# Optimization experiments

Hardware: AMD Instinct MI355X
Metric: run time of the kernel (lower is better)

The kernel has to match this reference:

```python
import jax, jax.numpy as jnp
import numpy as np

N = 50000
E = 800000
D = 64


def setup_inputs() -> dict:
    key = jax.random.key(0)
    k1, k2, k3, k4, k5, k6 = jax.random.split(key, 6)
    node_feats = jax.random.normal(k1, (N, D), dtype=jnp.float32)
    edge_feats = jax.random.normal(k2, (E, D), dtype=jnp.float32)
    src = jax.random.randint(k3, (E,), 0, N, dtype=jnp.int32)
    dst = jnp.sort(jax.random.randint(k4, (E,), 0, N, dtype=jnp.int32))
    # Linear(in_feats=D, out_feats=D) parameters (PyTorch default init scale)
    lim = 1.0 / np.sqrt(D)
    W = jax.random.uniform(k5, (D, D), minval=-lim, maxval=lim, dtype=jnp.float32)
    b = jax.random.uniform(k6, (D,), minval=-lim, maxval=lim, dtype=jnp.float32)
    return {"node_feats": node_feats, "edge_feats": edge_feats, "src": src,
            "dst": dst, "W": W, "b": b}


def reference(node_feats, edge_feats, src, dst, W, b):
    # u_add_e: per-edge message m_e = h_src(e) + h_e   [E, D]
    m = node_feats[src] + edge_feats
    # edge_softmax over edges grouped by destination node, per feature dim
    seg_max = jax.ops.segment_max(m, dst, num_segments=N)        # [N, D]
    seg_max = jnp.where(jnp.isfinite(seg_max), seg_max, 0.0)     # nodes w/o in-edges
    ex = jnp.exp(m - seg_max[dst])                               # [E, D]
    denom = jax.ops.segment_sum(ex, dst, num_segments=N)         # [N, D]
    a = ex / jnp.maximum(denom[dst], 1e-38)                      # [E, D]
    # weighted scatter-sum: h'_v = sum_{e->v} m_e * a_e
    agg = jax.ops.segment_sum(m * a, dst, num_segments=N)        # [N, D]
    # MLP + activation + residual (dropout=0, output_norm='none')
    out = jax.nn.relu(agg @ W.T + b) + node_feats
    return out
```

## Files before the change

### kernel.cpp

```cpp
#include <hip/hip_runtime.h>
#include <math.h>

#define DD 64
typedef float v4f __attribute__((ext_vector_type(4)));

__global__ __launch_bounds__(256) void prep_kernel(const int* __restrict__ dst,
                                                   int* __restrict__ row_start,
                                                   int N, int E) {
    int e = blockIdx.x * blockDim.x + threadIdx.x;
    if (e >= E) return;
    const int b = dst[e];
    const int a = (e == 0) ? -1 : dst[e - 1];
    for (int v = a + 1; v <= b; ++v) row_start[v] = e;
    if (e == E - 1) {
        for (int v = b + 1; v <= N; ++v) row_start[v] = E;
    }
}

__global__ __launch_bounds__(256) void fused_kernel(
    const float* __restrict__ node_feats,
    const float* __restrict__ edge_feats,
    const int*   __restrict__ src,
    const int*   __restrict__ row_start,
    const float* __restrict__ W,
    const float* __restrict__ bvec,
    float*       __restrict__ out,
    int N)
{
    __shared__ float rowbuf[4][DD];

    const int wave = threadIdx.x >> 6;
    const int lane = threadIdx.x & 63;
    const int grp  = lane >> 4;
    const int qd   = lane & 15;
    const int v = blockIdx.x * 4 + wave;
    if (v >= N) return;

    v4f wreg[16];
#pragma unroll
    for (int q = 0; q < 16; ++q)
        wreg[q] = ((const v4f*)W)[(size_t)lane * 16 + q];
    const float bj = bvec[lane];

    const int e0 = row_start[v];
    const int e1 = row_start[v + 1];

    const v4f* __restrict__ nf4 = (const v4f*)node_feats;
    const v4f* __restrict__ ef4 = (const v4f*)edge_feats;

    v4f se = {0.f, 0.f, 0.f, 0.f};
    v4f sm = {0.f, 0.f, 0.f, 0.f};

#define ACCUM(mv, valid)                                \
    {   v4f x;                                          \
        x.x = (valid) ? __expf((mv).x) : 0.f;           \
        x.y = (valid) ? __expf((mv).y) : 0.f;           \
        x.z = (valid) ? __expf((mv).z) : 0.f;           \
        x.w = (valid) ? __expf((mv).w) : 0.f;           \
        se += x;                                        \
        sm += (mv) * x;                                 \
    }

    for (int cb = e0; cb < e1; cb += 64) {
        const int li   = cb + lane;
        const int spre = src[li < e1 ? li : e0];
        const int cend = (cb + 64 < e1) ? (cb + 64) : e1;

        for (int eb = cb; eb < cend; eb += 16) {
            const int rb = eb - cb;
            const int sA = __shfl(spre, rb + grp,      64);
            const int sB = __shfl(spre, rb + 4  + grp, 64);
            const int sC = __shfl(spre, rb + 8  + grp, 64);
            const int sD = __shfl(spre, rb + 12 + grp, 64);

            const int eA = eb + grp,      eB = eb + 4 + grp;
            const int eC = eb + 8 + grp,  eD = eb + 12 + grp;
            const bool vA = eA < cend, vB = eB < cend;
            const bool vC = eC < cend, vD = eD < cend;
            const int cA = vA ? eA : e0, cB = vB ? eB : e0;
            const int cC = vC ? eC : e0, cD = vD ? eD : e0;

            const v4f gA = __builtin_nontemporal_load(ef4 + (size_t)cA * 16 + qd);
            const v4f gB = __builtin_nontemporal_load(ef4 + (size_t)cB * 16 + qd);
            const v4f gC = __builtin_nontemporal_load(ef4 + (size_t)cC * 16 + qd);
            const v4f gD = __builtin_nontemporal_load(ef4 + (size_t)cD * 16 + qd);
            const v4f nA = nf4[(size_t)sA * 16 + qd];
            const v4f nB = nf4[(size_t)sB * 16 + qd];
            const v4f nC = nf4[(size_t)sC * 16 + qd];
            const v4f nD = nf4[(size_t)sD * 16 + qd];

            const v4f mA = nA + gA;
            const v4f mB = nB + gB;
            const v4f mC = nC + gC;
            const v4f mD = nD + gD;
            ACCUM(mA, vA);
            ACCUM(mB, vB);
            ACCUM(mC, vC);
            ACCUM(mD, vD);
        }
    }
#undef ACCUM

    for (int off = 16; off < 64; off <<= 1) {
        se.x += __shfl_xor(se.x, off, 64);
        se.y += __shfl_xor(se.y, off, 64);
        se.z += __shfl_xor(se.z, off, 64);
        se.w += __shfl_xor(se.w, off, 64);
        sm.x += __shfl_xor(sm.x, off, 64);
        sm.y += __shfl_xor(sm.y, off, 64);
        sm.z += __shfl_xor(sm.z, off, 64);
        sm.w += __shfl_xor(sm.w, off, 64);
    }

    v4f a;
    a.x = sm.x / fmaxf(se.x, 1e-38f);
    a.y = sm.y / fmaxf(se.y, 1e-38f);
    a.z = sm.z / fmaxf(se.z, 1e-38f);
    a.w = sm.w / fmaxf(se.w, 1e-38f);

    if (grp == 0)
        *(v4f*)(&rowbuf[wave][qd * 4]) = a;
    asm volatile("s_waitcnt lgkmcnt(0)" ::: "memory");

    float acc = bj;
    const v4f* __restrict__ rp = (const v4f*)rowbuf[wave];
#pragma unroll
    for (int q = 0; q < 16; ++q) {
        const v4f av = rp[q];
        acc = fmaf(av.x, wreg[q].x, acc);
        acc = fmaf(av.y, wreg[q].y, acc);
        acc = fmaf(av.z, wreg[q].z, acc);
        acc = fmaf(av.w, wreg[q].w, acc);
    }
    const float res = node_feats[(size_t)v * DD + lane];
    out[(size_t)v * DD + lane] = fmaxf(acc, 0.f) + res;
}

extern "C" void kernel_launch(void* const* d_in, const int* in_sizes, int n_in,
                              void* d_out, int out_size, void* d_ws, size_t ws_size,
                              hipStream_t stream) {
    const float* node_feats = (const float*)d_in[0];
    const float* edge_feats = (const float*)d_in[1];
    const int*   src        = (const int*)  d_in[2];
    const int*   dst        = (const int*)  d_in[3];
    const float* W          = (const float*)d_in[4];
    const float* bvec       = (const float*)d_in[5];
    float*       out        = (float*)d_out;

    const int N = in_sizes[0] / DD;
    const int E = in_sizes[2];

    int* row_start = (int*)d_ws;

    {
        int blocks = (E + 255) / 256;
        prep_kernel<<<blocks, 256, 0, stream>>>(dst, row_start, N, E);
    }
    {
        int blocks = (N + 3) / 4;
        fused_kernel<<<blocks, 256, 0, stream>>>(node_feats, edge_feats, src,
                                                 row_start, W, bvec, out, N);
    }
}
```

Measured before the change: 376.3 us.

## Make fused kernel persistent with grid-stride nodes and prefetch next node's indices

Turns the fused aggregation kernel into a persistent grid-stride loop capped at 2048 blocks. Each wave loads W into registers once and reuses it across many nodes, and it prefetches row_start and the first src chunk for the next node while working on the current one. A launch-bounds occupancy hint is added. This amortizes the per-node W loads and hides index-load latency, at the cost of fewer resident waves and possible load imbalance across degree-varying nodes.

```diff
diff --git a/kernel.cpp b/kernel.cpp
--- a/kernel.cpp
+++ b/kernel.cpp
@@ -17,7 +17,7 @@
     }
 }
 
-__global__ __launch_bounds__(256) void fused_kernel(
+__global__ __launch_bounds__(256, 3) void fused_kernel(
     const float* __restrict__ node_feats,
     const float* __restrict__ edge_feats,
     const int*   __restrict__ src,
@@ -29,27 +29,33 @@
 {
     __shared__ float rowbuf[4][DD];
 
-    const int wave = threadIdx.x >> 6;
-    const int lane = threadIdx.x & 63;
-    const int grp  = lane >> 4;
-    const int qd   = lane & 15;
-    const int v = blockIdx.x * 4 + wave;
-    if (v >= N) return;
+    const int wave   = threadIdx.x >> 6;
+    const int lane   = threadIdx.x & 63;
+    const int grp    = lane >> 4;
+    const int qd     = lane & 15;
+    const int stride = gridDim.x * 4;
 
     v4f wreg[16];
 #pragma unroll
-    for (int q = 0; q < 16; ++q)
+    for (int q = 0; q < 16; ++q) {
         wreg[q] = ((const v4f*)W)[(size_t)lane * 16 + q];
+        asm volatile("" : "+v"(wreg[q]));
+    }
     const float bj = bvec[lane];
 
-    const int e0 = row_start[v];
-    const int e1 = row_start[v + 1];
+    int v = blockIdx.x * 4 + wave;
+    if (v >= N) return;
 
     const v4f* __restrict__ nf4 = (const v4f*)node_feats;
     const v4f* __restrict__ ef4 = (const v4f*)edge_feats;
 
-    v4f se = {0.f, 0.f, 0.f, 0.f};
-    v4f sm = {0.f, 0.f, 0.f, 0.f};
+    int e0 = row_start[v];
+    int e1 = row_start[v + 1];
+    int vn = v + stride;
+    int e0n = 0, e1n = 0;
+    if (vn < N) { e0n = row_start[vn]; e1n = row_start[vn + 1]; }
+    int li0 = e0 + lane;
+    int sc  = src[li0 < e1 ? li0 : (e1 > e0 ? e0 : 0)];
 
 #define ACCUM(mv, valid)                                \
     {   v4f x;                                          \
@@ -61,79 +67,100 @@
         sm += (mv) * x;                                 \
     }
 
-    for (int cb = e0; cb < e1; cb += 64) {
-        const int li   = cb + lane;
-        const int spre = src[li < e1 ? li : e0];
-        const int cend = (cb + 64 < e1) ? (cb + 64) : e1;
+    while (v < N) {
+        int spre_next = 0;
+        if (vn < N) {
+            const int lin = e0n + lane;
+            spre_next = src[lin < e1n ? lin : (e1n > e0n ? e0n : 0)];
+        }
+        const int v2 = vn + stride;
+        int e0nn = 0, e1nn = 0;
+        if (v2 < N) { e0nn = row_start[v2]; e1nn = row_start[v2 + 1]; }
 
-        for (int eb = cb; eb < cend; eb += 16) {
-            const int rb = eb - cb;
-            const int sA = __shfl(spre, rb + grp,      64);
-            const int sB = __shfl(spre, rb + 4  + grp, 64);
-            const int sC = __shfl(spre, rb + 8  + grp, 64);
-            const int sD = __shfl(spre, rb + 12 + grp, 64);
+        const float res = node_feats[(size_t)v * DD + lane];
 
-            const int eA = eb + grp,      eB = eb + 4 + grp;
-            const int eC = eb + 8 + grp,  eD = eb + 12 + grp;
-            const bool vA = eA < cend, vB = eB < cend;
-            const bool vC = eC < cend, vD = eD < cend;
-            const int cA = vA ? eA : e0, cB = vB ? eB : e0;
-            const int cC = vC ? eC : e0, cD = vD ? eD : e0;
+        v4f se = {0.f, 0.f, 0.f, 0.f};
+        v4f sm = {0.f, 0.f, 0.f, 0.f};
 
-            const v4f gA = __builtin_nontemporal_load(ef4 + (size_t)cA * 16 + qd);
-            const v4f gB = __builtin_nontemporal_load(ef4 + (size_t)cB * 16 + qd);
-            const v4f gC = __builtin_nontemporal_load(ef4 + (size_t)cC * 16 + qd);
-            const v4f gD = __builtin_nontemporal_load(ef4 + (size_t)cD * 16 + qd);
-            const v4f nA = nf4[(size_t)sA * 16 + qd];
-            const v4f nB = nf4[(size_t)sB * 16 + qd];
-            const v4f nC = nf4[(size_t)sC * 16 + qd];
-            const v4f nD = nf4[(size_t)sD * 16 + qd];
+        for (int cb = e0; cb < e1; cb += 64) {
+            const int li   = cb + lane;
+            const int spre = (cb == e0) ? sc
+                             : src[li < e1 ? li : e0];
+            const int cend = (cb + 64 < e1) ? (cb + 64) : e1;
 
-            const v4f mA = nA + gA;
-            const v4f mB = nB + gB;
-            const v4f mC = nC + gC;
-            const v4f mD = nD + gD;
-            ACCUM(mA, vA);
-            ACCUM(mB, vB);
-            ACCUM(mC, vC);
-            ACCUM(mD, vD);
+            for (int eb = cb; eb < cend; eb += 16) {
+                const int rb = eb - cb;
+                const int sA = __shfl(spre, rb + grp,      64);
+                const int sB = __shfl(spre, rb + 4  + grp, 64);
+                const int sC = __shfl(spre, rb + 8  + grp, 64);
+                const int sD = __shfl(spre, rb + 12 + grp, 64);
+
+                const int eA = eb + grp,      eB = eb + 4 + grp;
+                const int eC = eb + 8 + grp,  eD = eb + 12 + grp;
+                const bool vA = eA < cend, vB = eB < cend;
+                const bool vC = eC < cend, vD = eD < cend;
+                const int cA = vA ? eA : e0, cB = vB ? eB : e0;
+                const int cC = vC ? eC : e0, cD = vD ? eD : e0;
+
+                const v4f gA = __builtin_nontemporal_load(ef4 + (size_t)cA * 16 + qd);
+                const v4f gB = __builtin_nontemporal_load(ef4 + (size_t)cB * 16 + qd);
+                const v4f gC = __builtin_nontemporal_load(ef4 + (size_t)cC * 16 + qd);
+                const v4f gD = __builtin_nontemporal_load(ef4 + (size_t)cD * 16 + qd);
+                const v4f nA = nf4[(size_t)sA * 16 + qd];
+                const v4f nB = nf4[(size_t)sB * 16 + qd];
+                const v4f nC = nf4[(size_t)sC * 16 + qd];
+                const v4f nD = nf4[(size_t)sD * 16 + qd];
+
+                const v4f mA = nA + gA;
+                const v4f mB = nB + gB;
+                const v4f mC = nC + gC;
+                const v4f mD = nD + gD;
+                ACCUM(mA, vA);
+                ACCUM(mB, vB);
+                ACCUM(mC, vC);
+                ACCUM(mD, vD);
+            }
         }
+
+        for (int off = 16; off < 64; off <<= 1) {
+            se.x += __shfl_xor(se.x, off, 64);
+            se.y += __shfl_xor(se.y, off, 64);
+            se.z += __shfl_xor(se.z, off, 64);
+            se.w += __shfl_xor(se.w, off, 64);
+            sm.x += __shfl_xor(sm.x, off, 64);
+            sm.y += __shfl_xor(sm.y, off, 64);
+            sm.z += __shfl_xor(sm.z, off, 64);
+            sm.w += __shfl_xor(sm.w, off, 64);
+        }
+
+        v4f a;
+        a.x = sm.x / fmaxf(se.x, 1e-38f);
+        a.y = sm.y / fmaxf(se.y, 1e-38f);
+        a.z = sm.z / fmaxf(se.z, 1e-38f);
+        a.w = sm.w / fmaxf(se.w, 1e-38f);
+
+        if (grp == 0)
+            *(v4f*)(&rowbuf[wave][qd * 4]) = a;
+        asm volatile("s_waitcnt lgkmcnt(0)" ::: "memory");
+
+        float acc = bj;
+        const v4f* __restrict__ rp = (const v4f*)rowbuf[wave];
+#pragma unroll
+        for (int q = 0; q < 16; ++q) {
+            const v4f av = rp[q];
+            acc = fmaf(av.x, wreg[q].x, acc);
+            acc = fmaf(av.y, wreg[q].y, acc);
+            acc = fmaf(av.z, wreg[q].z, acc);
+            acc = fmaf(av.w, wreg[q].w, acc);
+        }
+        out[(size_t)v * DD + lane] = fmaxf(acc, 0.f) + res;
+
+        v  = vn;   vn  = v2;
+        e0 = e0n;  e1  = e1n;
+        e0n = e0nn; e1n = e1nn;
+        sc = spre_next;
     }
 #undef ACCUM
-
-    for (int off = 16; off < 64; off <<= 1) {
-        se.x += __shfl_xor(se.x, off, 64);
-        se.y += __shfl_xor(se.y, off, 64);
-        se.z += __shfl_xor(se.z, off, 64);
-        se.w += __shfl_xor(se.w, off, 64);
-        sm.x += __shfl_xor(sm.x, off, 64);
-        sm.y += __shfl_xor(sm.y, off, 64);
-        sm.z += __shfl_xor(sm.z, off, 64);
-        sm.w += __shfl_xor(sm.w, off, 64);
-    }
-
-    v4f a;
-    a.x = sm.x / fmaxf(se.x, 1e-38f);
-    a.y = sm.y / fmaxf(se.y, 1e-38f);
-    a.z = sm.z / fmaxf(se.z, 1e-38f);
-    a.w = sm.w / fmaxf(se.w, 1e-38f);
-
-    if (grp == 0)
-        *(v4f*)(&rowbuf[wave][qd * 4]) = a;
-    asm volatile("s_waitcnt lgkmcnt(0)" ::: "memory");
-
-    float acc = bj;
-    const v4f* __restrict__ rp = (const v4f*)rowbuf[wave];
-#pragma unroll
-    for (int q = 0; q < 16; ++q) {
-        const v4f av = rp[q];
-        acc = fmaf(av.x, wreg[q].x, acc);
-        acc = fmaf(av.y, wreg[q].y, acc);
-        acc = fmaf(av.z, wreg[q].z, acc);
-        acc = fmaf(av.w, wreg[q].w, acc);
-    }
-    const float res = node_feats[(size_t)v * DD + lane];
-    out[(size_t)v * DD + lane] = fmaxf(acc, 0.f) + res;
 }
 
 extern "C" void kernel_launch(void* const* d_in, const int* in_sizes, int n_in,
@@ -157,7 +184,8 @@
         prep_kernel<<<blocks, 256, 0, stream>>>(dst, row_start, N, E);
     }
     {
-        int blocks = (N + 3) / 4;
+        int maxb = (N + 3) / 4;
+        int blocks = maxb < 2048 ? maxb : 2048;
         fused_kernel<<<blocks, 256, 0, stream>>>(node_feats, edge_feats, src,
                                                  row_start, W, bvec, out, N);
     }
```

New measurement: 331.0 us. -12.1%, faster.
